# Performance work log

Measured on AMD Instinct MI355X. Metric: run time of the kernel, lower is better.

The kernel has to match this reference:

```python
import jax, jax.numpy as jnp
import numpy as np

DT = 0.02  # Settings.TIMESTEP_PLANNER default
N_CONTROLS = 2  # angular_control, translational_control (first 2 input indices)
N_STATES = 7    # remaining inputs are state variables, outputs are their D_ derivatives


def setup_inputs() -> dict:
    key = jax.random.key(0)
    ks = jax.random.split(key, 4)
    B, H, F, Hid = 32768, 50, 9, 256
    scale = 0.1
    return {
        "x": jax.random.normal(ks[0], (B, H, F), dtype=jnp.float32),
        "W1": jax.random.normal(ks[1], (F, Hid), dtype=jnp.float32) * scale,
        "b1": jnp.zeros((Hid,), dtype=jnp.float32),
        "W2": jax.random.normal(ks[2], (Hid, Hid), dtype=jnp.float32) * scale,
        "b2": jnp.zeros((Hid,), dtype=jnp.float32),
        "W3": jax.random.normal(ks[3], (Hid, N_STATES), dtype=jnp.float32) * scale,
        "b3": jnp.zeros((N_STATES,), dtype=jnp.float32),
    }


def reference(x, W1, b1, W2, b2, W3, b3):
    # gather initial state (state input indices are 2..8) and control sequence (indices 0,1)
    state0 = x[:, 0, N_CONTROLS:]          # [B, 7]
    controls = x[:, :, :N_CONTROLS]        # [B, H, 2]

    def mlp(inp):
        h = jnp.tanh(inp @ W1 + b1)
        h = jnp.tanh(h @ W2 + b2)
        return h @ W3 + b3                 # [B, 7] derivative outputs D_*

    def step(state, u_t):
        # scatter: assemble net input in original input ordering [controls, states]
        net_in = jnp.concatenate([u_t, state], axis=1)   # [B, 9]
        d_state = mlp(net_in)
        new_state = state + DT * d_state                 # differential Euler update
        return new_state, new_state

    u_seq = jnp.swapaxes(controls, 0, 1)                 # [H, B, 2]
    _, outs = jax.lax.scan(step, state0, u_seq)          # [H, B, 7]
    return jnp.swapaxes(outs, 0, 1)                      # [B, H, 7]
```

## Files before the change

### kernel.cpp

```cpp
#include <hip/hip_runtime.h>
#include <hip/hip_bf16.h>

constexpr int HID = 256;
constexpr int NS = 7, NC = 2, NF = 9, HS = 50;
constexpr int BT  = 32;
constexpr int ROW = 264;
constexpr int NIP = 40;
constexpr float DT_C = 0.02f;

using short8 = __attribute__((ext_vector_type(8))) short;
using f32x4  = __attribute__((ext_vector_type(4))) float;

__device__ __forceinline__ unsigned short f2bf(float f) {
    unsigned int u = __float_as_uint(f);
    return (unsigned short)((u + 0x7FFFu + ((u >> 16) & 1u)) >> 16);
}
__device__ __forceinline__ unsigned int pk2(float lo, float hi) {
    __hip_bfloat162 h = __float22bfloat162_rn(make_float2(lo, hi));
    return *reinterpret_cast<unsigned int*>(&h);
}
__device__ __forceinline__ float fast_tanh(float x) {
    float e = __expf(2.0f * x);
    return fmaf(-2.0f, __builtin_amdgcn_rcpf(e + 1.0f), 1.0f);
}

__global__ __launch_bounds__(512, 4)
void rollout_mfma7(const float* __restrict__ x,
                   const float* __restrict__ W1, const float* __restrict__ b1,
                   const float* __restrict__ W2, const float* __restrict__ b2,
                   const float* __restrict__ W3, const float* __restrict__ b3,
                   float* __restrict__ out)
{
    __shared__ __align__(16) unsigned short h[BT][ROW];
    __shared__ __align__(16) unsigned short w3t[16][ROW];
    __shared__ __align__(16) unsigned short nibf[BT][NIP];
    __shared__ __align__(16) float b2s[HID];

    const int tid  = threadIdx.x;
    const int w    = tid >> 6;
    const int lane = tid & 63;
    const int l15  = lane & 15;
    const int lg   = lane >> 4;
    const int b0   = blockIdx.x * BT;

    short8 w2f[2][8];
    #pragma unroll
    for (int q = 0; q < 2; ++q) {
        const int n = w * 32 + q * 16 + l15;
        #pragma unroll
        for (int kb = 0; kb < 8; ++kb)
            #pragma unroll
            for (int j = 0; j < 8; ++j)
                w2f[q][kb][j] = (short)f2bf(W2[(kb * 32 + lg * 8 + j) * HID + n]);
    }
    short8 w1f[2];
    #pragma unroll
    for (int q = 0; q < 2; ++q) {
        const int n = w * 32 + q * 16 + l15;
        #pragma unroll
        for (int j = 0; j < 8; ++j) {
            const int k = lg * 8 + j;
            float v = (k < NF) ? W1[k * HID + n] : (k == NF ? b1[n] : 0.0f);
            w1f[q][j] = (short)f2bf(v);
        }
    }
    float b3r[4];
    #pragma unroll
    for (int r = 0; r < 4; ++r) {
        const int s = lg * 4 + r;
        b3r[r] = (s < NS) ? b3[s] : 0.0f;
    }
    for (int i = tid; i < HID; i += 512) b2s[i] = b2[i];
    for (int i = tid; i < 16 * HID; i += 512) {
        const int s = i & 15, k = i >> 4;
        w3t[s][k] = (s < NS) ? f2bf(W3[k * NS + s]) : (unsigned short)0;
    }
    if (tid < BT) {
        const float* xp = &x[(b0 + tid) * (HS * NF)];
        #pragma unroll
        for (int k = 0; k < NIP; ++k) nibf[tid][k] = 0;
        #pragma unroll
        for (int f = 0; f < NF; ++f) nibf[tid][f] = f2bf(xp[f]);
        nibf[tid][NF] = f2bf(1.0f);
    }
    float st[4] = {0.f, 0.f, 0.f, 0.f};
    if (w < 2) {
        const int b = w * 16 + l15;
        #pragma unroll
        for (int r = 0; r < 4; ++r) {
            const int s = lg * 4 + r;
            if (s < NS) st[r] = x[(b0 + b) * (HS * NF) + NC + s];
        }
    }
    __syncthreads();

    for (int t = 0; t < HS; ++t) {
        f32x4 a1[2][2];
        #pragma unroll
        for (int q = 0; q < 2; ++q) { a1[q][0] = {0,0,0,0}; a1[q][1] = {0,0,0,0}; }
        #pragma unroll
        for (int bt = 0; bt < 2; ++bt) {
            short8 nf = *reinterpret_cast<const short8*>(&nibf[bt * 16 + l15][lg * 8]);
            #pragma unroll
            for (int q = 0; q < 2; ++q)
                a1[q][bt] = __builtin_amdgcn_mfma_f32_16x16x32_bf16(w1f[q], nf, a1[q][bt], 0, 0, 0);
        }
        #pragma unroll
        for (int q = 0; q < 2; ++q)
            #pragma unroll
            for (int bt = 0; bt < 2; ++bt) {
                uint2 pk;
                pk.x = pk2(fast_tanh(a1[q][bt][0]), fast_tanh(a1[q][bt][1]));
                pk.y = pk2(fast_tanh(a1[q][bt][2]), fast_tanh(a1[q][bt][3]));
                *reinterpret_cast<uint2*>(&h[bt * 16 + l15][w * 32 + q * 16 + lg * 4]) = pk;
            }
        __syncthreads();

        f32x4 acc[2][2];
        #pragma unroll
        for (int q = 0; q < 2; ++q) {
            const float4 bv = *reinterpret_cast<const float4*>(&b2s[w * 32 + q * 16 + lg * 4]);
            f32x4 bi; bi[0] = bv.x; bi[1] = bv.y; bi[2] = bv.z; bi[3] = bv.w;
            acc[q][0] = bi; acc[q][1] = bi;
        }
        #pragma unroll
        for (int kb = 0; kb < 8; ++kb) {
            short8 h0  = *reinterpret_cast<const short8*>(&h[l15][kb * 32 + lg * 8]);
            short8 h1v = *reinterpret_cast<const short8*>(&h[16 + l15][kb * 32 + lg * 8]);
            #pragma unroll
            for (int q = 0; q < 2; ++q) {
                acc[q][0] = __builtin_amdgcn_mfma_f32_16x16x32_bf16(w2f[q][kb], h0,  acc[q][0], 0, 0, 0);
                acc[q][1] = __builtin_amdgcn_mfma_f32_16x16x32_bf16(w2f[q][kb], h1v, acc[q][1], 0, 0, 0);
            }
        }
        uint2 pkv[2][2];
        #pragma unroll
        for (int q = 0; q < 2; ++q)
            #pragma unroll
            for (int bt = 0; bt < 2; ++bt) {
                pkv[q][bt].x = pk2(fast_tanh(acc[q][bt][0]), fast_tanh(acc[q][bt][1]));
                pkv[q][bt].y = pk2(fast_tanh(acc[q][bt][2]), fast_tanh(acc[q][bt][3]));
            }
        __syncthreads();

        #pragma unroll
        for (int q = 0; q < 2; ++q)
            #pragma unroll
            for (int bt = 0; bt < 2; ++bt)
                *reinterpret_cast<uint2*>(&h[bt * 16 + l15][w * 32 + q * 16 + lg * 4]) = pkv[q][bt];
        __syncthreads();

        if (w < 2) {
            f32x4 a3 = {0.f, 0.f, 0.f, 0.f};
            #pragma unroll
            for (int kb = 0; kb < 8; ++kb) {
                short8 hv = *reinterpret_cast<const short8*>(&h[w * 16 + l15][kb * 32 + lg * 8]);
                short8 wf = *reinterpret_cast<const short8*>(&w3t[l15][kb * 32 + lg * 8]);
                a3 = __builtin_amdgcn_mfma_f32_16x16x32_bf16(wf, hv, a3, 0, 0, 0);
            }
            const int b = w * 16 + l15;
            float nsv[4];
            #pragma unroll
            for (int r = 0; r < 4; ++r) nsv[r] = st[r] + DT_C * (a3[r] + b3r[r]);
            if (lg == 0) {
                st[0] = nsv[0]; st[1] = nsv[1]; st[2] = nsv[2]; st[3] = nsv[3];
                *reinterpret_cast<unsigned int*>(&nibf[b][2]) = pk2(nsv[0], nsv[1]);
                *reinterpret_cast<unsigned int*>(&nibf[b][4]) = pk2(nsv[2], nsv[3]);
                const int obase = (b0 + b) * (HS * NS) + t * NS;
                out[obase + 0] = nsv[0];
                out[obase + 1] = nsv[1];
                out[obase + 2] = nsv[2];
                out[obase + 3] = nsv[3];
            } else if (lg == 1) {
                st[0] = nsv[0]; st[1] = nsv[1]; st[2] = nsv[2];
                *reinterpret_cast<unsigned int*>(&nibf[b][6]) = pk2(nsv[0], nsv[1]);
                nibf[b][8] = (unsigned short)pk2(nsv[2], nsv[2]);
                const int obase = (b0 + b) * (HS * NS) + t * NS;
                out[obase + 4] = nsv[0];
                out[obase + 5] = nsv[1];
                out[obase + 6] = nsv[2];
            }
        } else if (w == 2) {
            if (t + 1 < HS) {
                const int b = lane & 31, c = lane >> 5;
                nibf[b][c] = f2bf(x[(b0 + b) * (HS * NF) + (t + 1) * NF + c]);
            }
        }
        __syncthreads();
    }
}

extern "C" void kernel_launch(void* const* d_in, const int* in_sizes, int n_in,
                              void* d_out, int out_size, void* d_ws, size_t ws_size,
                              hipStream_t stream) {
    const float* x  = (const float*)d_in[0];
    const float* W1 = (const float*)d_in[1];
    const float* b1 = (const float*)d_in[2];
    const float* W2 = (const float*)d_in[3];
    const float* b2 = (const float*)d_in[4];
    const float* W3 = (const float*)d_in[5];
    const float* b3 = (const float*)d_in[6];
    float* out = (float*)d_out;

    const int B = in_sizes[0] / (HS * NF);
    dim3 grid(B / BT), block(512);
    hipLaunchKernelGGL(rollout_mfma7, grid, block, 0, stream,
                       x, W1, b1, W2, b2, W3, b3, out);
}
```

Before: 410.5 us.

## Stream pre-transposed bf16 W2 from global instead of holding it in registers

A small pre-kernel transposes W2 and converts it to bf16 in the workspace. The main kernel then loads W2 fragments from global/L2 on every timestep instead of keeping 64 VGPRs of W2 per lane. This frees registers so the launch bound can rise from 4 to 8 blocks per SM for higher occupancy. The cost is repeated global/L2 reads of W2 every step, an extra launch, and a fallback path used when the workspace is too small.

```diff
diff --git a/kernel.cpp b/kernel.cpp
--- a/kernel.cpp
+++ b/kernel.cpp
@@ -24,10 +24,21 @@
     return fmaf(-2.0f, __builtin_amdgcn_rcpf(e + 1.0f), 1.0f);
 }
 
-__global__ __launch_bounds__(512, 4)
-void rollout_mfma7(const float* __restrict__ x,
+__global__ void transpose_w2(const float* __restrict__ W2,
+                             unsigned short* __restrict__ w2t)
+{
+    __shared__ float tile[32][33];
+    const int tx = threadIdx.x, ty = threadIdx.y;
+    const int bx = blockIdx.x & 7, by = blockIdx.x >> 3;
+    tile[ty][tx] = W2[(by * 32 + ty) * HID + bx * 32 + tx];
+    __syncthreads();
+    w2t[(bx * 32 + ty) * HID + by * 32 + tx] = f2bf(tile[tx][ty]);
+}
+
+__global__ __launch_bounds__(512, 8)
+void rollout_mfma8(const float* __restrict__ x,
                    const float* __restrict__ W1, const float* __restrict__ b1,
-                   const float* __restrict__ W2, const float* __restrict__ b2,
+                   const unsigned short* __restrict__ w2t, const float* __restrict__ b2,
                    const float* __restrict__ W3, const float* __restrict__ b3,
                    float* __restrict__ out)
 {
@@ -43,16 +54,10 @@
     const int lg   = lane >> 4;
     const int b0   = blockIdx.x * BT;
 
-    short8 w2f[2][8];
-    #pragma unroll
-    for (int q = 0; q < 2; ++q) {
-        const int n = w * 32 + q * 16 + l15;
-        #pragma unroll
-        for (int kb = 0; kb < 8; ++kb)
-            #pragma unroll
-            for (int j = 0; j < 8; ++j)
-                w2f[q][kb][j] = (short)f2bf(W2[(kb * 32 + lg * 8 + j) * HID + n]);
-    }
+    const int i0 = (w * 32 + l15) * HID + lg * 8;
+    const short8* wq0 = reinterpret_cast<const short8*>(w2t + i0);
+    const short8* wq1 = reinterpret_cast<const short8*>(w2t + i0 + 16 * HID);
+
     short8 w1f[2];
     #pragma unroll
     for (int q = 0; q < 2; ++q) {
@@ -123,15 +128,16 @@
             f32x4 bi; bi[0] = bv.x; bi[1] = bv.y; bi[2] = bv.z; bi[3] = bv.w;
             acc[q][0] = bi; acc[q][1] = bi;
         }
-        #pragma unroll
+        #pragma unroll 2
         for (int kb = 0; kb < 8; ++kb) {
+            short8 f0  = wq0[kb * 4];
+            short8 f1  = wq1[kb * 4];
             short8 h0  = *reinterpret_cast<const short8*>(&h[l15][kb * 32 + lg * 8]);
             short8 h1v = *reinterpret_cast<const short8*>(&h[16 + l15][kb * 32 + lg * 8]);
-            #pragma unroll
-            for (int q = 0; q < 2; ++q) {
-                acc[q][0] = __builtin_amdgcn_mfma_f32_16x16x32_bf16(w2f[q][kb], h0,  acc[q][0], 0, 0, 0);
-                acc[q][1] = __builtin_amdgcn_mfma_f32_16x16x32_bf16(w2f[q][kb], h1v, acc[q][1], 0, 0, 0);
-            }
+            acc[0][0] = __builtin_amdgcn_mfma_f32_16x16x32_bf16(f0, h0,  acc[0][0], 0, 0, 0);
+            acc[0][1] = __builtin_amdgcn_mfma_f32_16x16x32_bf16(f0, h1v, acc[0][1], 0, 0, 0);
+            acc[1][0] = __builtin_amdgcn_mfma_f32_16x16x32_bf16(f1, h0,  acc[1][0], 0, 0, 0);
+            acc[1][1] = __builtin_amdgcn_mfma_f32_16x16x32_bf16(f1, h1v, acc[1][1], 0, 0, 0);
         }
         uint2 pkv[2][2];
         #pragma unroll
@@ -190,6 +196,172 @@
     }
 }
 
+__global__ __launch_bounds__(512, 4)
+void rollout_mfma7(const float* __restrict__ x,
+                   const float* __restrict__ W1, const float* __restrict__ b1,
+                   const float* __restrict__ W2, const float* __restrict__ b2,
+                   const float* __restrict__ W3, const float* __restrict__ b3,
+                   float* __restrict__ out)
+{
+    __shared__ __align__(16) unsigned short h[BT][ROW];
+    __shared__ __align__(16) unsigned short w3t[16][ROW];
+    __shared__ __align__(16) unsigned short nibf[BT][NIP];
+    __shared__ __align__(16) float b2s[HID];
+
+    const int tid  = threadIdx.x;
+    const int w    = tid >> 6;
+    const int lane = tid & 63;
+    const int l15  = lane & 15;
+    const int lg   = lane >> 4;
+    const int b0   = blockIdx.x * BT;
+
+    short8 w2f[2][8];
+    #pragma unroll
+    for (int q = 0; q < 2; ++q) {
+        const int n = w * 32 + q * 16 + l15;
+        #pragma unroll
+        for (int kb = 0; kb < 8; ++kb)
+            #pragma unroll
+            for (int j = 0; j < 8; ++j)
+                w2f[q][kb][j] = (short)f2bf(W2[(kb * 32 + lg * 8 + j) * HID + n]);
+    }
+    short8 w1f[2];
+    #pragma unroll
+    for (int q = 0; q < 2; ++q) {
+        const int n = w * 32 + q * 16 + l15;
+        #pragma unroll
+        for (int j = 0; j < 8; ++j) {
+            const int k = lg * 8 + j;
+            float v = (k < NF) ? W1[k * HID + n] : (k == NF ? b1[n] : 0.0f);
+            w1f[q][j] = (short)f2bf(v);
+        }
+    }
+    float b3r[4];
+    #pragma unroll
+    for (int r = 0; r < 4; ++r) {
+        const int s = lg * 4 + r;
+        b3r[r] = (s < NS) ? b3[s] : 0.0f;
+    }
+    for (int i = tid; i < HID; i += 512) b2s[i] = b2[i];
+    for (int i = tid; i < 16 * HID; i += 512) {
+        const int s = i & 15, k = i >> 4;
+        w3t[s][k] = (s < NS) ? f2bf(W3[k * NS + s]) : (unsigned short)0;
+    }
+    if (tid < BT) {
+        const float* xp = &x[(b0 + tid) * (HS * NF)];
+        #pragma unroll
+        for (int k = 0; k < NIP; ++k) nibf[tid][k] = 0;
+        #pragma unroll
+        for (int f = 0; f < NF; ++f) nibf[tid][f] = f2bf(xp[f]);
+        nibf[tid][NF] = f2bf(1.0f);
+    }
+    float st[4] = {0.f, 0.f, 0.f, 0.f};
+    if (w < 2) {
+        const int b = w * 16 + l15;
+        #pragma unroll
+        for (int r = 0; r < 4; ++r) {
+            const int s = lg * 4 + r;
+            if (s < NS) st[r] = x[(b0 + b) * (HS * NF) + NC + s];
+        }
+    }
+    __syncthreads();
+
+    for (int t = 0; t < HS; ++t) {
+        f32x4 a1[2][2];
+        #pragma unroll
+        for (int q = 0; q < 2; ++q) { a1[q][0] = {0,0,0,0}; a1[q][1] = {0,0,0,0}; }
+        #pragma unroll
+        for (int bt = 0; bt < 2; ++bt) {
+            short8 nf = *reinterpret_cast<const short8*>(&nibf[bt * 16 + l15][lg * 8]);
+            #pragma unroll
+            for (int q = 0; q < 2; ++q)
+                a1[q][bt] = __builtin_amdgcn_mfma_f32_16x16x32_bf16(w1f[q], nf, a1[q][bt], 0, 0, 0);
+        }
+        #pragma unroll
+        for (int q = 0; q < 2; ++q)
+            #pragma unroll
+            for (int bt = 0; bt < 2; ++bt) {
+                uint2 pk;
+                pk.x = pk2(fast_tanh(a1[q][bt][0]), fast_tanh(a1[q][bt][1]));
+                pk.y = pk2(fast_tanh(a1[q][bt][2]), fast_tanh(a1[q][bt][3]));
+                *reinterpret_cast<uint2*>(&h[bt * 16 + l15][w * 32 + q * 16 + lg * 4]) = pk;
+            }
+        __syncthreads();
+
+        f32x4 acc[2][2];
+        #pragma unroll
+        for (int q = 0; q < 2; ++q) {
+            const float4 bv = *reinterpret_cast<const float4*>(&b2s[w * 32 + q * 16 + lg * 4]);
+            f32x4 bi; bi[0] = bv.x; bi[1] = bv.y; bi[2] = bv.z; bi[3] = bv.w;
+            acc[q][0] = bi; acc[q][1] = bi;
+        }
+        #pragma unroll
+        for (int kb = 0; kb < 8; ++kb) {
+            short8 h0  = *reinterpret_cast<const short8*>(&h[l15][kb * 32 + lg * 8]);
+            short8 h1v = *reinterpret_cast<const short8*>(&h[16 + l15][kb * 32 + lg * 8]);
+            #pragma unroll
+            for (int q = 0; q < 2; ++q) {
+                acc[q][0] = __builtin_amdgcn_mfma_f32_16x16x32_bf16(w2f[q][kb], h0,  acc[q][0], 0, 0, 0);
+                acc[q][1] = __builtin_amdgcn_mfma_f32_16x16x32_bf16(w2f[q][kb], h1v, acc[q][1], 0, 0, 0);
+            }
+        }
+        uint2 pkv[2][2];
+        #pragma unroll
+        for (int q = 0; q < 2; ++q)
+            #pragma unroll
+            for (int bt = 0; bt < 2; ++bt) {
+                pkv[q][bt].x = pk2(fast_tanh(acc[q][bt][0]), fast_tanh(acc[q][bt][1]));
+                pkv[q][bt].y = pk2(fast_tanh(acc[q][bt][2]), fast_tanh(acc[q][bt][3]));
+            }
+        __syncthreads();
+
+        #pragma unroll
+        for (int q = 0; q < 2; ++q)
+            #pragma unroll
+            for (int bt = 0; bt < 2; ++bt)
+                *reinterpret_cast<uint2*>(&h[bt * 16 + l15][w * 32 + q * 16 + lg * 4]) = pkv[q][bt];
+        __syncthreads();
+
+        if (w < 2) {
+            f32x4 a3 = {0.f, 0.f, 0.f, 0.f};
+            #pragma unroll
+            for (int kb = 0; kb < 8; ++kb) {
+                short8 hv = *reinterpret_cast<const short8*>(&h[w * 16 + l15][kb * 32 + lg * 8]);
+                short8 wf = *reinterpret_cast<const short8*>(&w3t[l15][kb * 32 + lg * 8]);
+                a3 = __builtin_amdgcn_mfma_f32_16x16x32_bf16(wf, hv, a3, 0, 0, 0);
+            }
+            const int b = w * 16 + l15;
+            float nsv[4];
+            #pragma unroll
+            for (int r = 0; r < 4; ++r) nsv[r] = st[r] + DT_C * (a3[r] + b3r[r]);
+            if (lg == 0) {
+                st[0] = nsv[0]; st[1] = nsv[1]; st[2] = nsv[2]; st[3] = nsv[3];
+                *reinterpret_cast<unsigned int*>(&nibf[b][2]) = pk2(nsv[0], nsv[1]);
+                *reinterpret_cast<unsigned int*>(&nibf[b][4]) = pk2(nsv[2], nsv[3]);
+                const int obase = (b0 + b) * (HS * NS) + t * NS;
+                out[obase + 0] = nsv[0];
+                out[obase + 1] = nsv[1];
+                out[obase + 2] = nsv[2];
+                out[obase + 3] = nsv[3];
+            } else if (lg == 1) {
+                st[0] = nsv[0]; st[1] = nsv[1]; st[2] = nsv[2];
+                *reinterpret_cast<unsigned int*>(&nibf[b][6]) = pk2(nsv[0], nsv[1]);
+                nibf[b][8] = (unsigned short)pk2(nsv[2], nsv[2]);
+                const int obase = (b0 + b) * (HS * NS) + t * NS;
+                out[obase + 4] = nsv[0];
+                out[obase + 5] = nsv[1];
+                out[obase + 6] = nsv[2];
+            }
+        } else if (w == 2) {
+            if (t + 1 < HS) {
+                const int b = lane & 31, c = lane >> 5;
+                nibf[b][c] = f2bf(x[(b0 + b) * (HS * NF) + (t + 1) * NF + c]);
+            }
+        }
+        __syncthreads();
+    }
+}
+
 extern "C" void kernel_launch(void* const* d_in, const int* in_sizes, int n_in,
                               void* d_out, int out_size, void* d_ws, size_t ws_size,
                               hipStream_t stream) {
@@ -204,6 +376,14 @@
 
     const int B = in_sizes[0] / (HS * NF);
     dim3 grid(B / BT), block(512);
-    hipLaunchKernelGGL(rollout_mfma7, grid, block, 0, stream,
-                       x, W1, b1, W2, b2, W3, b3, out);
-}
+
+    if (ws_size >= (size_t)(HID * HID * sizeof(unsigned short))) {
+        unsigned short* w2t = (unsigned short*)d_ws;
+        hipLaunchKernelGGL(transpose_w2, dim3(64), dim3(32, 32), 0, stream, W2, w2t);
+        hipLaunchKernelGGL(rollout_mfma8, grid, block, 0, stream,
+                           x, W1, b1, w2t, b2, W3, b3, out);
+    } else {
+        hipLaunchKernelGGL(rollout_mfma7, grid, block, 0, stream,
+                           x, W1, b1, W2, b2, W3, b3, out);
+    }
+}
```

Measured after the change: 725.9 us. 1.77x slower.

## Split hidden dimension across 16 waves with 1024-thread blocks

Applied to the files above, without the earlier changes.

Blocks grow from 8 to 16 wavefronts, and each wave now owns 16 hidden columns of W1/W2 instead of 32. This halves the register-resident W2 fragments and the MFMA work per wave, which should raise occupancy and latency hiding in the serial per-timestep loop. In exchange, each wave re-reads the full h tile from LDS for half the MFMAs, and more waves join each block-wide barrier. The layer-3 and state-update code is unchanged, so most of the extra waves sit idle during that phase.

```diff
diff --git a/kernel.cpp b/kernel.cpp
--- a/kernel.cpp
+++ b/kernel.cpp
@@ -24,8 +24,8 @@
     return fmaf(-2.0f, __builtin_amdgcn_rcpf(e + 1.0f), 1.0f);
 }
 
-__global__ __launch_bounds__(512, 4)
-void rollout_mfma7(const float* __restrict__ x,
+__global__ __launch_bounds__(1024, 8)
+void rollout_mfma9(const float* __restrict__ x,
                    const float* __restrict__ W1, const float* __restrict__ b1,
                    const float* __restrict__ W2, const float* __restrict__ b2,
                    const float* __restrict__ W3, const float* __restrict__ b3,
@@ -43,25 +43,23 @@
     const int lg   = lane >> 4;
     const int b0   = blockIdx.x * BT;
 
-    short8 w2f[2][8];
-    #pragma unroll
-    for (int q = 0; q < 2; ++q) {
-        const int n = w * 32 + q * 16 + l15;
+    short8 w2f[8];
+    {
+        const int n = w * 16 + l15;
         #pragma unroll
         for (int kb = 0; kb < 8; ++kb)
             #pragma unroll
             for (int j = 0; j < 8; ++j)
-                w2f[q][kb][j] = (short)f2bf(W2[(kb * 32 + lg * 8 + j) * HID + n]);
+                w2f[kb][j] = (short)f2bf(W2[(kb * 32 + lg * 8 + j) * HID + n]);
     }
-    short8 w1f[2];
-    #pragma unroll
-    for (int q = 0; q < 2; ++q) {
-        const int n = w * 32 + q * 16 + l15;
+    short8 w1f;
+    {
+        const int n = w * 16 + l15;
         #pragma unroll
         for (int j = 0; j < 8; ++j) {
             const int k = lg * 8 + j;
             float v = (k < NF) ? W1[k * HID + n] : (k == NF ? b1[n] : 0.0f);
-            w1f[q][j] = (short)f2bf(v);
+            w1f[j] = (short)f2bf(v);
         }
     }
     float b3r[4];
@@ -70,8 +68,8 @@
         const int s = lg * 4 + r;
         b3r[r] = (s < NS) ? b3[s] : 0.0f;
     }
-    for (int i = tid; i < HID; i += 512) b2s[i] = b2[i];
-    for (int i = tid; i < 16 * HID; i += 512) {
+    for (int i = tid; i < HID; i += 1024) b2s[i] = b2[i];
+    for (int i = tid; i < 16 * HID; i += 1024) {
         const int s = i & 15, k = i >> 4;
         w3t[s][k] = (s < NS) ? f2bf(W3[k * NS + s]) : (unsigned short)0;
     }
@@ -95,59 +93,51 @@
     __syncthreads();
 
     for (int t = 0; t < HS; ++t) {
-        f32x4 a1[2][2];
-        #pragma unroll
-        for (int q = 0; q < 2; ++q) { a1[q][0] = {0,0,0,0}; a1[q][1] = {0,0,0,0}; }
-        #pragma unroll
-        for (int bt = 0; bt < 2; ++bt) {
-            short8 nf = *reinterpret_cast<const short8*>(&nibf[bt * 16 + l15][lg * 8]);
+        {
+            f32x4 a1[2];
+            a1[0] = {0, 0, 0, 0};
+            a1[1] = {0, 0, 0, 0};
             #pragma unroll
-            for (int q = 0; q < 2; ++q)
-                a1[q][bt] = __builtin_amdgcn_mfma_f32_16x16x32_bf16(w1f[q], nf, a1[q][bt], 0, 0, 0);
-        }
-        #pragma unroll
-        for (int q = 0; q < 2; ++q)
+            for (int bt = 0; bt < 2; ++bt) {
+                short8 nf = *reinterpret_cast<const short8*>(&nibf[bt * 16 + l15][lg * 8]);
+                a1[bt] = __builtin_amdgcn_mfma_f32_16x16x32_bf16(w1f, nf, a1[bt], 0, 0, 0);
+            }
             #pragma unroll
             for (int bt = 0; bt < 2; ++bt) {
                 uint2 pk;
-                pk.x = pk2(fast_tanh(a1[q][bt][0]), fast_tanh(a1[q][bt][1]));
-                pk.y = pk2(fast_tanh(a1[q][bt][2]), fast_tanh(a1[q][bt][3]));
-                *reinterpret_cast<uint2*>(&h[bt * 16 + l15][w * 32 + q * 16 + lg * 4]) = pk;
+                pk.x = pk2(fast_tanh(a1[bt][0]), fast_tanh(a1[bt][1]));
+                pk.y = pk2(fast_tanh(a1[bt][2]), fast_tanh(a1[bt][3]));
+                *reinterpret_cast<uint2*>(&h[bt * 16 + l15][w * 16 + lg * 4]) = pk;
             }
+        }
         __syncthreads();
 
-        f32x4 acc[2][2];
-        #pragma unroll
-        for (int q = 0; q < 2; ++q) {
-            const float4 bv = *reinterpret_cast<const float4*>(&b2s[w * 32 + q * 16 + lg * 4]);
-            f32x4 bi; bi[0] = bv.x; bi[1] = bv.y; bi[2] = bv.z; bi[3] = bv.w;
-            acc[q][0] = bi; acc[q][1] = bi;
-        }
-        #pragma unroll
-        for (int kb = 0; kb < 8; ++kb) {
-            short8 h0  = *reinterpret_cast<const short8*>(&h[l15][kb * 32 + lg * 8]);
-            short8 h1v = *reinterpret_cast<const short8*>(&h[16 + l15][kb * 32 + lg * 8]);
+        uint2 pkv[2];
+        {
+            f32x4 acc[2];
+            {
+                const float4 bv = *reinterpret_cast<const float4*>(&b2s[w * 16 + lg * 4]);
+                f32x4 bi; bi[0] = bv.x; bi[1] = bv.y; bi[2] = bv.z; bi[3] = bv.w;
+                acc[0] = bi; acc[1] = bi;
+            }
             #pragma unroll
-            for (int q = 0; q < 2; ++q) {
-                acc[q][0] = __builtin_amdgcn_mfma_f32_16x16x32_bf16(w2f[q][kb], h0,  acc[q][0], 0, 0, 0);
-                acc[q][1] = __builtin_amdgcn_mfma_f32_16x16x32_bf16(w2f[q][kb], h1v, acc[q][1], 0, 0, 0);
+            for (int kb = 0; kb < 8; ++kb) {
+                short8 h0  = *reinterpret_cast<const short8*>(&h[l15][kb * 32 + lg * 8]);
+                short8 h1v = *reinterpret_cast<const short8*>(&h[16 + l15][kb * 32 + lg * 8]);
+                acc[0] = __builtin_amdgcn_mfma_f32_16x16x32_bf16(w2f[kb], h0,  acc[0], 0, 0, 0);
+                acc[1] = __builtin_amdgcn_mfma_f32_16x16x32_bf16(w2f[kb], h1v, acc[1], 0, 0, 0);
+            }
+            #pragma unroll
+            for (int bt = 0; bt < 2; ++bt) {
+                pkv[bt].x = pk2(fast_tanh(acc[bt][0]), fast_tanh(acc[bt][1]));
+                pkv[bt].y = pk2(fast_tanh(acc[bt][2]), fast_tanh(acc[bt][3]));
             }
         }
-        uint2 pkv[2][2];
-        #pragma unroll
-        for (int q = 0; q < 2; ++q)
-            #pragma unroll
-            for (int bt = 0; bt < 2; ++bt) {
-                pkv[q][bt].x = pk2(fast_tanh(acc[q][bt][0]), fast_tanh(acc[q][bt][1]));
-                pkv[q][bt].y = pk2(fast_tanh(acc[q][bt][2]), fast_tanh(acc[q][bt][3]));
-            }
         __syncthreads();
 
         #pragma unroll
-        for (int q = 0; q < 2; ++q)
-            #pragma unroll
-            for (int bt = 0; bt < 2; ++bt)
-                *reinterpret_cast<uint2*>(&h[bt * 16 + l15][w * 32 + q * 16 + lg * 4]) = pkv[q][bt];
+        for (int bt = 0; bt < 2; ++bt)
+            *reinterpret_cast<uint2*>(&h[bt * 16 + l15][w * 16 + lg * 4]) = pkv[bt];
         __syncthreads();
 
         if (w < 2) {
@@ -203,7 +193,7 @@
     float* out = (float*)d_out;
 
     const int B = in_sizes[0] / (HS * NF);
-    dim3 grid(B / BT), block(512);
-    hipLaunchKernelGGL(rollout_mfma7, grid, block, 0, stream,
+    dim3 grid(B / BT), block(1024);
+    hipLaunchKernelGGL(rollout_mfma9, grid, block, 0, stream,
                        x, W1, b1, W2, b2, W3, b3, out);
 }
```

Result: slower. 463.4 us (+12.9%).

## Process 64 batch rows per block to amortize register-resident weights and barriers

Applied to the files above, without the earlier changes.

Doubles the batch tile per block from 32 to 64 rows. The layer-2 MFMA loop now runs over two 32-row tiles that reuse the same register-held W2 fragments. Layer 1, layer 3 and the control prefetch are remapped to cover 64 rows, using four waves for the output layer and wave 4 for prefetch. This halves the number of blocks and the per-timestep barrier count per row, and folds DT*b3 into a shared constant. In exchange it uses more LDS and registers per block, launches fewer blocks, and leaves more waves idle during the serial layer-3 phase.

```diff
diff --git a/kernel.cpp b/kernel.cpp
--- a/kernel.cpp
+++ b/kernel.cpp
@@ -3,9 +3,9 @@
 
 constexpr int HID = 256;
 constexpr int NS = 7, NC = 2, NF = 9, HS = 50;
-constexpr int BT  = 32;
+constexpr int BT  = 64;
 constexpr int ROW = 264;
-constexpr int NIP = 40;
+constexpr int NIP = 32;
 constexpr float DT_C = 0.02f;
 
 using short8 = __attribute__((ext_vector_type(8))) short;
@@ -25,16 +25,17 @@
 }
 
 __global__ __launch_bounds__(512, 4)
-void rollout_mfma7(const float* __restrict__ x,
-                   const float* __restrict__ W1, const float* __restrict__ b1,
-                   const float* __restrict__ W2, const float* __restrict__ b2,
-                   const float* __restrict__ W3, const float* __restrict__ b3,
-                   float* __restrict__ out)
+void rollout_mfma11(const float* __restrict__ x,
+                    const float* __restrict__ W1, const float* __restrict__ b1,
+                    const float* __restrict__ W2, const float* __restrict__ b2,
+                    const float* __restrict__ W3, const float* __restrict__ b3,
+                    float* __restrict__ out)
 {
     __shared__ __align__(16) unsigned short h[BT][ROW];
     __shared__ __align__(16) unsigned short w3t[16][ROW];
     __shared__ __align__(16) unsigned short nibf[BT][NIP];
     __shared__ __align__(16) float b2s[HID];
+    __shared__ __align__(16) float db3[16];
 
     const int tid  = threadIdx.x;
     const int w    = tid >> 6;
@@ -64,13 +65,8 @@
             w1f[q][j] = (short)f2bf(v);
         }
     }
-    float b3r[4];
-    #pragma unroll
-    for (int r = 0; r < 4; ++r) {
-        const int s = lg * 4 + r;
-        b3r[r] = (s < NS) ? b3[s] : 0.0f;
-    }
     for (int i = tid; i < HID; i += 512) b2s[i] = b2[i];
+    if (tid < 16) db3[tid] = (tid < NS) ? DT_C * b3[tid] : 0.0f;
     for (int i = tid; i < 16 * HID; i += 512) {
         const int s = i & 15, k = i >> 4;
         w3t[s][k] = (s < NS) ? f2bf(W3[k * NS + s]) : (unsigned short)0;
@@ -84,8 +80,8 @@
         nibf[tid][NF] = f2bf(1.0f);
     }
     float st[4] = {0.f, 0.f, 0.f, 0.f};
-    if (w < 2) {
-        const int b = w * 16 + l15;
+    if (w < 4) {
+        const int b = (w >> 1) * 32 + (w & 1) * 16 + l15;
         #pragma unroll
         for (int r = 0; r < 4; ++r) {
             const int s = lg * 4 + r;
@@ -95,73 +91,77 @@
     __syncthreads();
 
     for (int t = 0; t < HS; ++t) {
-        f32x4 a1[2][2];
-        #pragma unroll
-        for (int q = 0; q < 2; ++q) { a1[q][0] = {0,0,0,0}; a1[q][1] = {0,0,0,0}; }
-        #pragma unroll
-        for (int bt = 0; bt < 2; ++bt) {
-            short8 nf = *reinterpret_cast<const short8*>(&nibf[bt * 16 + l15][lg * 8]);
+        #pragma unroll
+        for (int rt = 0; rt < 4; ++rt) {
+            f32x4 a1 = {0.f, 0.f, 0.f, 0.f};
+            short8 nf = *reinterpret_cast<const short8*>(&nibf[rt * 16 + l15][lg * 8]);
+            f32x4 a1b = __builtin_amdgcn_mfma_f32_16x16x32_bf16(w1f[0], nf, a1, 0, 0, 0);
+            f32x4 a1c = __builtin_amdgcn_mfma_f32_16x16x32_bf16(w1f[1], nf, a1, 0, 0, 0);
+            uint2 pk0, pk1;
+            pk0.x = pk2(fast_tanh(a1b[0]), fast_tanh(a1b[1]));
+            pk0.y = pk2(fast_tanh(a1b[2]), fast_tanh(a1b[3]));
+            pk1.x = pk2(fast_tanh(a1c[0]), fast_tanh(a1c[1]));
+            pk1.y = pk2(fast_tanh(a1c[2]), fast_tanh(a1c[3]));
+            *reinterpret_cast<uint2*>(&h[rt * 16 + l15][w * 32 + lg * 4]) = pk0;
+            *reinterpret_cast<uint2*>(&h[rt * 16 + l15][w * 32 + 16 + lg * 4]) = pk1;
+        }
+        __syncthreads();
+
+        uint2 pkvA[4], pkvB[4];
+        #pragma unroll
+        for (int tile = 0; tile < 2; ++tile) {
+            f32x4 acc[2][2];
+            #pragma unroll
+            for (int q = 0; q < 2; ++q) {
+                const float4 bv = *reinterpret_cast<const float4*>(&b2s[w * 32 + q * 16 + lg * 4]);
+                f32x4 bi; bi[0] = bv.x; bi[1] = bv.y; bi[2] = bv.z; bi[3] = bv.w;
+                acc[q][0] = bi; acc[q][1] = bi;
+            }
+            #pragma unroll
+            for (int kb = 0; kb < 8; ++kb) {
+                short8 h0  = *reinterpret_cast<const short8*>(&h[tile * 32 + l15][kb * 32 + lg * 8]);
+                short8 h1v = *reinterpret_cast<const short8*>(&h[tile * 32 + 16 + l15][kb * 32 + lg * 8]);
+                #pragma unroll
+                for (int q = 0; q < 2; ++q) {
+                    acc[q][0] = __builtin_amdgcn_mfma_f32_16x16x32_bf16(w2f[q][kb], h0,  acc[q][0], 0, 0, 0);
+                    acc[q][1] = __builtin_amdgcn_mfma_f32_16x16x32_bf16(w2f[q][kb], h1v, acc[q][1], 0, 0, 0);
+                }
+            }
+            uint2* pkv = tile ? pkvB : pkvA;
             #pragma unroll
             for (int q = 0; q < 2; ++q)
-                a1[q][bt] = __builtin_amdgcn_mfma_f32_16x16x32_bf16(w1f[q], nf, a1[q][bt], 0, 0, 0);
-        }
+                #pragma unroll
+                for (int bt = 0; bt < 2; ++bt) {
+                    pkv[q * 2 + bt].x = pk2(fast_tanh(acc[q][bt][0]), fast_tanh(acc[q][bt][1]));
+                    pkv[q * 2 + bt].y = pk2(fast_tanh(acc[q][bt][2]), fast_tanh(acc[q][bt][3]));
+                }
+        }
+        __syncthreads();
+
         #pragma unroll
         for (int q = 0; q < 2; ++q)
             #pragma unroll
             for (int bt = 0; bt < 2; ++bt) {
-                uint2 pk;
-                pk.x = pk2(fast_tanh(a1[q][bt][0]), fast_tanh(a1[q][bt][1]));
-                pk.y = pk2(fast_tanh(a1[q][bt][2]), fast_tanh(a1[q][bt][3]));
-                *reinterpret_cast<uint2*>(&h[bt * 16 + l15][w * 32 + q * 16 + lg * 4]) = pk;
-            }
-        __syncthreads();
-
-        f32x4 acc[2][2];
-        #pragma unroll
-        for (int q = 0; q < 2; ++q) {
-            const float4 bv = *reinterpret_cast<const float4*>(&b2s[w * 32 + q * 16 + lg * 4]);
-            f32x4 bi; bi[0] = bv.x; bi[1] = bv.y; bi[2] = bv.z; bi[3] = bv.w;
-            acc[q][0] = bi; acc[q][1] = bi;
-        }
-        #pragma unroll
-        for (int kb = 0; kb < 8; ++kb) {
-            short8 h0  = *reinterpret_cast<const short8*>(&h[l15][kb * 32 + lg * 8]);
-            short8 h1v = *reinterpret_cast<const short8*>(&h[16 + l15][kb * 32 + lg * 8]);
-            #pragma unroll
-            for (int q = 0; q < 2; ++q) {
-                acc[q][0] = __builtin_amdgcn_mfma_f32_16x16x32_bf16(w2f[q][kb], h0,  acc[q][0], 0, 0, 0);
-                acc[q][1] = __builtin_amdgcn_mfma_f32_16x16x32_bf16(w2f[q][kb], h1v, acc[q][1], 0, 0, 0);
-            }
-        }
-        uint2 pkv[2][2];
-        #pragma unroll
-        for (int q = 0; q < 2; ++q)
-            #pragma unroll
-            for (int bt = 0; bt < 2; ++bt) {
-                pkv[q][bt].x = pk2(fast_tanh(acc[q][bt][0]), fast_tanh(acc[q][bt][1]));
-                pkv[q][bt].y = pk2(fast_tanh(acc[q][bt][2]), fast_tanh(acc[q][bt][3]));
-            }
-        __syncthreads();
-
-        #pragma unroll
-        for (int q = 0; q < 2; ++q)
-            #pragma unroll
-            for (int bt = 0; bt < 2; ++bt)
-                *reinterpret_cast<uint2*>(&h[bt * 16 + l15][w * 32 + q * 16 + lg * 4]) = pkv[q][bt];
-        __syncthreads();
-
-        if (w < 2) {
+                *reinterpret_cast<uint2*>(&h[bt * 16 + l15][w * 32 + q * 16 + lg * 4]) = pkvA[q * 2 + bt];
+                *reinterpret_cast<uint2*>(&h[32 + bt * 16 + l15][w * 32 + q * 16 + lg * 4]) = pkvB[q * 2 + bt];
+            }
+        __syncthreads();
+
+        if (w < 4) {
+            const int b = (w >> 1) * 32 + (w & 1) * 16 + l15;
             f32x4 a3 = {0.f, 0.f, 0.f, 0.f};
             #pragma unroll
             for (int kb = 0; kb < 8; ++kb) {
-                short8 hv = *reinterpret_cast<const short8*>(&h[w * 16 + l15][kb * 32 + lg * 8]);
+                short8 hv = *reinterpret_cast<const short8*>(&h[b][kb * 32 + lg * 8]);
                 short8 wf = *reinterpret_cast<const short8*>(&w3t[l15][kb * 32 + lg * 8]);
                 a3 = __builtin_amdgcn_mfma_f32_16x16x32_bf16(wf, hv, a3, 0, 0, 0);
             }
-            const int b = w * 16 + l15;
+            const float4 d3 = *reinterpret_cast<const float4*>(&db3[lg * 4]);
             float nsv[4];
-            #pragma unroll
-            for (int r = 0; r < 4; ++r) nsv[r] = st[r] + DT_C * (a3[r] + b3r[r]);
+            nsv[0] = st[0] + DT_C * a3[0] + d3.x;
+            nsv[1] = st[1] + DT_C * a3[1] + d3.y;
+            nsv[2] = st[2] + DT_C * a3[2] + d3.z;
+            nsv[3] = st[3] + DT_C * a3[3] + d3.w;
             if (lg == 0) {
                 st[0] = nsv[0]; st[1] = nsv[1]; st[2] = nsv[2]; st[3] = nsv[3];
                 *reinterpret_cast<unsigned int*>(&nibf[b][2]) = pk2(nsv[0], nsv[1]);
@@ -180,10 +180,12 @@
                 out[obase + 5] = nsv[1];
                 out[obase + 6] = nsv[2];
             }
-        } else if (w == 2) {
+        } else if (w == 4) {
             if (t + 1 < HS) {
-                const int b = lane & 31, c = lane >> 5;
-                nibf[b][c] = f2bf(x[(b0 + b) * (HS * NF) + (t + 1) * NF + c]);
+                const int b = lane;
+                const float* xp = &x[(b0 + b) * (HS * NF) + (t + 1) * NF];
+                nibf[b][0] = f2bf(xp[0]);
+                nibf[b][1] = f2bf(xp[1]);
             }
         }
         __syncthreads();
@@ -204,6 +206,6 @@
 
     const int B = in_sizes[0] / (HS * NF);
     dim3 grid(B / BT), block(512);
-    hipLaunchKernelGGL(rollout_mfma7, grid, block, 0, stream,
+    hipLaunchKernelGGL(rollout_mfma11, grid, block, 0, stream,
                        x, W1, b1, W2, b2, W3, b3, out);
 }
```

After: 370.2 us. -9.8%, faster.
